# Kernel tuning notes

Hardware: AMD Instinct MI355X
Metric: run time of the kernel (lower is better)

## Reference

```python
import jax, jax.numpy as jnp
import numpy as np

N_NODES = 50000
N_EDGES = 500000
F_IN = 128
HID = 160      # hidden_sf * model_dim = 5 * 32
F_OUT = 128    # out_sf * output_channels = 4 * 32
N_GRAPHS = 50
OUT_DIM = 10


def setup_inputs() -> dict:
    key = jax.random.key(0)
    ks = jax.random.split(key, 16)
    x = jax.random.normal(ks[0], (N_NODES, F_IN), dtype=jnp.float32)
    edge_index = jax.random.randint(ks[1], (2, N_EDGES), 0, N_NODES, dtype=jnp.int64)
    batch = jnp.sort(jax.random.randint(ks[2], (N_NODES,), 0, N_GRAPHS, dtype=jnp.int64))

    def lin(k, fi, fo):
        return jax.random.normal(k, (fi, fo), dtype=jnp.float32) * (1.0 / np.sqrt(fi))

    dims = [(F_IN, HID), (HID, HID), (HID, HID), (HID, F_OUT)]
    params = {}
    for i, (fi, fo) in enumerate(dims):
        params[f"W{i}"] = lin(ks[3 + i], fi, fo)
        params[f"b{i}"] = jnp.zeros((fo,), dtype=jnp.float32)
    params["fc_w"] = lin(ks[8], F_OUT, OUT_DIM)
    params["fc_b"] = jnp.zeros((OUT_DIM,), dtype=jnp.float32)
    return {"x": x, "edge_index": edge_index, "batch": batch, **params}


def _gcn_layer(x, W, b, src, dst, dinv):
    # PyG GCNConv (improved=True): x' = D^{-1/2}(A + 2I)D^{-1/2} X W + b
    xw = x @ W                                   # [N, F_out]
    norm = dinv[src] * dinv[dst]                 # [E]
    msgs = xw[src] * norm[:, None]               # [E, F_out] gather
    agg = jax.ops.segment_sum(msgs, dst, num_segments=N_NODES)  # scatter-add
    # self-loop contribution with fill value 2 (improved)
    agg = agg + (2.0 * dinv * dinv)[:, None] * xw
    return agg + b


def reference(x, edge_index, batch, W0, b0, W1, b1, W2, b2, W3, b3, fc_w, fc_b):
    src, dst = edge_index[0], edge_index[1]
    ones_e = jnp.ones((N_EDGES,), dtype=x.dtype)
    deg = jax.ops.segment_sum(ones_e, dst, num_segments=N_NODES) + 2.0
    dinv = jax.lax.rsqrt(deg)

    h = x
    for (W, b) in [(W0, b0), (W1, b1), (W2, b2), (W3, b3)]:
        h = _gcn_layer(h, W, b, src, dst, dinv)

    # global mean pool per graph
    sums = jax.ops.segment_sum(h, batch, num_segments=N_GRAPHS)        # [G, F_OUT]
    cnts = jax.ops.segment_sum(jnp.ones((N_NODES,), h.dtype), batch, num_segments=N_GRAPHS)
    pooled = sums / jnp.maximum(cnts, 1.0)[:, None]

    logits = pooled @ fc_w + fc_b
    return jax.nn.log_softmax(logits, axis=1)
```

## Files before the change

kernel.cpp:

```cpp
#include <hip/hip_runtime.h>

#define N_NODES 50000
#define N_EDGES 500000
#define F_IN    128
#define HID     160
#define NG      50
#define OUT_DIM 10
#define PC      16
#define MAXDEG  48
#define PADK    164
#define FSTRIDE 132

#define NRANGE  8
#define RNODES  (N_NODES / NRANGE)
#define FILLB   64
#define NPACK   (N_EDGES / 4)

#define XF_ROWS   32
#define XF_BLOCKS  ((N_NODES + XF_ROWS - 1) / XF_ROWS)
#define DINV_BLOCKS ((N_NODES + 255) / 256)

__global__ void k_pre(const int* __restrict__ src, const int* __restrict__ dst,
                      int* __restrict__ deg, int* __restrict__ ell,
                      const float* __restrict__ W0, const float* __restrict__ b0,
                      const float* __restrict__ W1, const float* __restrict__ b1,
                      const float* __restrict__ W2, const float* __restrict__ b2,
                      const float* __restrict__ W3, const float* __restrict__ b3,
                      const float* __restrict__ fcw, const int* __restrict__ batch,
                      float* __restrict__ Fmt, float* __restrict__ r0,
                      float* __restrict__ r1, float* __restrict__ r2,
                      float* __restrict__ r3, int* __restrict__ start) {
    const int t = threadIdx.x;
    if (blockIdx.x >= 2) {
        const int rb    = blockIdx.x - 2;
        const int range = rb & (NRANGE - 1);
        const int sub   = rb >> 3;
        const int lo    = range * RNODES;
        const int4* d4 = (const int4*)dst;
        const int4* s4 = (const int4*)src;
        for (int pk = sub * 256 + t; pk < NPACK; pk += FILLB * 256) {
            const int4 dv = d4[pk];
            const int4 sv = s4[pk];
            #pragma unroll
            for (int j = 0; j < 4; ++j) {
                const int d = (&dv.x)[j];
                if ((unsigned)(d - lo) < (unsigned)RNODES) {
                    int p = atomicAdd(&deg[d], 1);
                    if (p < MAXDEG) ell[d * MAXDEG + p] = (&sv.x)[j];
                }
            }
        }
        return;
    }
    if (blockIdx.x == 1) {
        int g = t;
        if (g > NG) return;
        int lo = 0, hi = N_NODES;
        while (lo < hi) {
            int mid = (lo + hi) >> 1;
            if (batch[mid] < g) lo = mid + 1; else hi = mid;
        }
        start[g] = lo;
        return;
    }
    __shared__ float sA[OUT_DIM * PADK];
    __shared__ float sB[OUT_DIM * PADK];
    float* cur = sA;
    float* nxt = sB;

    for (int idx = t; idx < F_IN * OUT_DIM; idx += 256) {
        int k = idx / OUT_DIM, c = idx - k * OUT_DIM;
        cur[c * PADK + k] = fcw[idx];
    }
    __syncthreads();
    if (t < OUT_DIM) {
        float acc = 0.f;
        const float4* Bv = (const float4*)b3;
        for (int k4 = 0; k4 < F_IN / 4; ++k4) {
            float4 w = Bv[k4];
            float4 b = *(const float4*)&cur[t * PADK + 4 * k4];
            acc += w.x * b.x + w.y * b.y + w.z * b.z + w.w * b.w;
        }
        r3[t] = acc;
    }
    __syncthreads();

    auto stage = [&](const float* __restrict__ W, const float* __restrict__ bias,
                     float* __restrict__ biasOut, int M, int K, bool toGlobal) {
        const int r = t;
        const bool isBias = (r == M) && (bias != nullptr);
        if (r < M || isBias) {
            const float* Arow = isBias ? bias : (W + r * K);
            const float4* Wv = (const float4*)Arow;
            float acc[OUT_DIM];
            #pragma unroll
            for (int c = 0; c < OUT_DIM; ++c) acc[c] = 0.f;
            #pragma unroll 4
            for (int k4 = 0; k4 < K / 4; ++k4) {
                float4 w = Wv[k4];
                #pragma unroll
                for (int c = 0; c < OUT_DIM; ++c) {
                    float4 b = *(const float4*)&cur[c * PADK + 4 * k4];
                    acc[c] += w.x * b.x + w.y * b.y + w.z * b.z + w.w * b.w;
                }
            }
            if (isBias) {
                #pragma unroll
                for (int c = 0; c < OUT_DIM; ++c) biasOut[c] = acc[c];
            } else if (toGlobal) {
                #pragma unroll
                for (int c = 0; c < OUT_DIM; ++c) Fmt[c * FSTRIDE + r] = acc[c];
            } else {
                #pragma unroll
                for (int c = 0; c < OUT_DIM; ++c) nxt[c * PADK + r] = acc[c];
            }
        }
        __syncthreads();
        float* tmp = cur; cur = nxt; nxt = tmp;
    };

    stage(W3, nullptr, nullptr, HID, F_IN, false);
    stage(W2, b2, r2, HID, HID, false);
    stage(W1, b1, r1, HID, HID, false);
    stage(W0, b0, r0, F_IN, HID, true);
}

__global__ void k_xf_dinv(const float* __restrict__ X, const float* __restrict__ Fmt,
                          const int* __restrict__ deg,
                          float* __restrict__ Y0, float* __restrict__ dinv) {
    const int t = threadIdx.x;
    if (blockIdx.x >= XF_BLOCKS) {
        int i = (blockIdx.x - XF_BLOCKS) * 256 + t;
        if (i < N_NODES) dinv[i] = rsqrtf((float)deg[i] + 2.0f);
        return;
    }
    __shared__ float sX[XF_ROWS][132];
    __shared__ float sFt[OUT_DIM * FSTRIDE];
    const int base = blockIdx.x * XF_ROWS;
    for (int idx = t; idx < XF_ROWS * F_IN; idx += 256) {
        int rr = idx >> 7, kk = idx & 127;
        int gr = base + rr;
        sX[rr][kk] = (gr < N_NODES) ? X[(size_t)gr * F_IN + kk] : 0.f;
    }
    for (int idx = t; idx < OUT_DIM * FSTRIDE; idx += 256) sFt[idx] = Fmt[idx];
    __syncthreads();
    const int r = t >> 4, c = t & 15;
    float a0 = 0.f, a1 = 0.f;
    if (c < OUT_DIM) {
        for (int k = 0; k < F_IN; k += 4) {
            const float4 x0 = *(const float4*)&sX[r][k];
            const float4 x1 = *(const float4*)&sX[r + 16][k];
            const float4 f  = *(const float4*)&sFt[c * FSTRIDE + k];
            a0 += x0.x * f.x + x0.y * f.y + x0.z * f.z + x0.w * f.w;
            a1 += x1.x * f.x + x1.y * f.y + x1.z * f.z + x1.w * f.w;
        }
    }
    const float pad = (c == 10) ? 1.0f : 0.0f;
    const float v0 = (c < OUT_DIM) ? a0 : pad;
    const float v1 = (c < OUT_DIM) ? a1 : pad;
    const int g0 = base + r, g1 = base + r + 16;
    if (g0 < N_NODES) Y0[(size_t)g0 * PC + c] = v0;
    if (g1 < N_NODES) Y0[(size_t)g1 * PC + c] = v1;
}

__global__ void k_prop16(const float* __restrict__ in, const float* __restrict__ dinv,
                         const int* __restrict__ deg, const int* __restrict__ ell,
                         float* __restrict__ out) {
    const int gid  = blockIdx.x * blockDim.x + threadIdx.x;
    const int i    = gid >> 6;
    const int lane = threadIdx.x & 63;
    const int esub = lane >> 4, c = lane & 15;
    int d = deg[i];
    const int dc = (d < MAXDEG) ? d : MAXDEG;
    float acc = 0.f;
    const int base = i * MAXDEG;
    for (int k = esub; k < dc; k += 4) {
        int s = ell[base + k];
        acc += dinv[s] * in[(size_t)s * PC + c];
    }
    acc += __shfl_xor(acc, 16);
    acc += __shfl_xor(acc, 32);
    if (lane < 16) {
        float di = dinv[i];
        out[(size_t)i * PC + c] = di * (acc + 2.0f * di * in[(size_t)i * PC + c]);
    }
}

__global__ void k_pool_final(const float* __restrict__ Y1, const float* __restrict__ Y2,
                             const float* __restrict__ Y3, const float* __restrict__ Y4,
                             const int* __restrict__ start,
                             const float* __restrict__ r0, const float* __restrict__ r1,
                             const float* __restrict__ r2, const float* __restrict__ r3,
                             const float* __restrict__ fcb, float* __restrict__ out) {
    const int g = blockIdx.x, t = threadIdx.x;
    __shared__ float red[256];
    __shared__ float S_sh[16];
    __shared__ float qsh[3];
    __shared__ float lg[OUT_DIM];
    const int st = start[g], cnt = start[g + 1] - st;
    const int c = t & 15, rr = t >> 4;

    float acc = 0.f;
    for (int r = rr; r < cnt; r += 16) acc += Y4[(size_t)(st + r) * PC + c];
    red[t] = acc; __syncthreads();
    if (t < 128) red[t] += red[t + 128]; __syncthreads();
    if (t < 64)  red[t] += red[t + 64];  __syncthreads();
    if (t < 32)  red[t] += red[t + 32];  __syncthreads();
    if (t < 16)  S_sh[t] = red[t] + red[t + 16];

    float a1 = 0.f, a2 = 0.f, a3 = 0.f;
    for (int r = t; r < cnt; r += 256) {
        a1 += Y1[(size_t)(st + r) * PC + 10];
        a2 += Y2[(size_t)(st + r) * PC + 10];
        a3 += Y3[(size_t)(st + r) * PC + 10];
    }
    __syncthreads(); red[t] = a1; __syncthreads();
    for (int o = 128; o > 0; o >>= 1) { if (t < o) red[t] += red[t + o]; __syncthreads(); }
    if (t == 0) qsh[0] = red[0];
    __syncthreads(); red[t] = a2; __syncthreads();
    for (int o = 128; o > 0; o >>= 1) { if (t < o) red[t] += red[t + o]; __syncthreads(); }
    if (t == 0) qsh[1] = red[0];
    __syncthreads(); red[t] = a3; __syncthreads();
    for (int o = 128; o > 0; o >>= 1) { if (t < o) red[t] += red[t + o]; __syncthreads(); }
    if (t == 0) qsh[2] = red[0];
    __syncthreads();

    if (t < OUT_DIM) {
        float n = (float)cnt; if (n < 1.f) n = 1.f;
        lg[t] = (S_sh[t] + qsh[2] * r0[t] + qsh[1] * r1[t] + qsh[0] * r2[t]) / n
                + r3[t] + fcb[t];
    }
    __syncthreads();
    if (t == 0) {
        float m = -1e30f;
        for (int o = 0; o < OUT_DIM; ++o) m = fmaxf(m, lg[o]);
        float ss = 0.f;
        for (int o = 0; o < OUT_DIM; ++o) ss += expf(lg[o] - m);
        float ls = logf(ss) + m;
        for (int o = 0; o < OUT_DIM; ++o) out[g * OUT_DIM + o] = lg[o] - ls;
    }
}

extern "C" void kernel_launch(void* const* d_in, const int* in_sizes, int n_in,
                              void* d_out, int out_size, void* d_ws, size_t ws_size,
                              hipStream_t stream) {
    const float* x     = (const float*)d_in[0];
    const int*   ei    = (const int*)d_in[1];
    const int*   src   = ei;
    const int*   dstp  = ei + N_EDGES;
    const int*   batch = (const int*)d_in[2];
    const float* W0 = (const float*)d_in[3];
    const float* b0 = (const float*)d_in[4];
    const float* W1 = (const float*)d_in[5];
    const float* b1 = (const float*)d_in[6];
    const float* W2 = (const float*)d_in[7];
    const float* b2 = (const float*)d_in[8];
    const float* W3 = (const float*)d_in[9];
    const float* b3 = (const float*)d_in[10];
    const float* fcw = (const float*)d_in[11];
    const float* fcb = (const float*)d_in[12];
    float* out = (float*)d_out;

    char* p = (char*)d_ws;
    auto alloc = [&](size_t bytes) -> void* {
        void* r = (void*)p;
        p += (bytes + 255) & ~(size_t)255;
        return r;
    };
    int*   deg   = (int*)alloc(N_NODES * 4);
    int*   start = (int*)alloc((NG + 1) * 4);
    float* dinv  = (float*)alloc(N_NODES * 4);
    int*   ell   = (int*)alloc((size_t)N_NODES * MAXDEG * 4);
    float* Fmt   = (float*)alloc(OUT_DIM * FSTRIDE * 4);
    float* r0    = (float*)alloc(OUT_DIM * 4);
    float* r1    = (float*)alloc(OUT_DIM * 4);
    float* r2    = (float*)alloc(OUT_DIM * 4);
    float* r3    = (float*)alloc(OUT_DIM * 4);
    float* Y0    = (float*)alloc((size_t)N_NODES * PC * 4);
    float* Y1    = (float*)alloc((size_t)N_NODES * PC * 4);
    float* Y2    = (float*)alloc((size_t)N_NODES * PC * 4);
    float* Y3    = (float*)alloc((size_t)N_NODES * PC * 4);
    float* Y4    = (float*)alloc((size_t)N_NODES * PC * 4);

    hipMemsetAsync(deg, 0, N_NODES * 4, stream);

    const int TB = 256;
    k_pre<<<NRANGE * FILLB + 2, TB, 0, stream>>>(src, dstp, deg, ell,
                                                 W0, b0, W1, b1, W2, b2, W3, b3,
                                                 fcw, batch, Fmt, r0, r1, r2, r3, start);
    k_xf_dinv<<<XF_BLOCKS + DINV_BLOCKS, TB, 0, stream>>>(x, Fmt, deg, Y0, dinv);

    const int PROP_BLOCKS = N_NODES * 64 / TB;
    k_prop16<<<PROP_BLOCKS, TB, 0, stream>>>(Y0, dinv, deg, ell, Y1);
    k_prop16<<<PROP_BLOCKS, TB, 0, stream>>>(Y1, dinv, deg, ell, Y2);
    k_prop16<<<PROP_BLOCKS, TB, 0, stream>>>(Y2, dinv, deg, ell, Y3);
    k_prop16<<<PROP_BLOCKS, TB, 0, stream>>>(Y3, dinv, deg, ell, Y4);

    k_pool_final<<<NG, TB, 0, stream>>>(Y1, Y2, Y3, Y4, start, r0, r1, r2, r3, fcb, out);
}
```

Before: 258.4 us.

## Restructure pre-pass: fold memset into init kernel, fuse ELL fill with X transform, recompute dinv

```diff
diff --git a/kernel.cpp b/kernel.cpp
--- a/kernel.cpp
+++ b/kernel.cpp
@@ -13,26 +13,109 @@
 
 #define NRANGE  8
 #define RNODES  (N_NODES / NRANGE)
-#define FILLB   64
+#define FILLB   128
+#define FB      (NRANGE * FILLB)
 #define NPACK   (N_EDGES / 4)
 
 #define XF_ROWS   32
-#define XF_BLOCKS  ((N_NODES + XF_ROWS - 1) / XF_ROWS)
-#define DINV_BLOCKS ((N_NODES + 255) / 256)
-
-__global__ void k_pre(const int* __restrict__ src, const int* __restrict__ dst,
-                      int* __restrict__ deg, int* __restrict__ ell,
-                      const float* __restrict__ W0, const float* __restrict__ b0,
-                      const float* __restrict__ W1, const float* __restrict__ b1,
-                      const float* __restrict__ W2, const float* __restrict__ b2,
-                      const float* __restrict__ W3, const float* __restrict__ b3,
-                      const float* __restrict__ fcw, const int* __restrict__ batch,
-                      float* __restrict__ Fmt, float* __restrict__ r0,
-                      float* __restrict__ r1, float* __restrict__ r2,
-                      float* __restrict__ r3, int* __restrict__ start) {
+#define XF_BLOCKS ((N_NODES + XF_ROWS - 1) / XF_ROWS)
+#define ZERO_BLOCKS ((N_NODES + 255) / 256)
+
+__global__ void k_init(const float* __restrict__ W0, const float* __restrict__ b0,
+                       const float* __restrict__ W1, const float* __restrict__ b1,
+                       const float* __restrict__ W2, const float* __restrict__ b2,
+                       const float* __restrict__ W3, const float* __restrict__ b3,
+                       const float* __restrict__ fcw, const int* __restrict__ batch,
+                       float* __restrict__ Fmt, float* __restrict__ r0,
+                       float* __restrict__ r1, float* __restrict__ r2,
+                       float* __restrict__ r3, int* __restrict__ start,
+                       int* __restrict__ deg) {
     const int t = threadIdx.x;
     if (blockIdx.x >= 2) {
-        const int rb    = blockIdx.x - 2;
+        int i = (blockIdx.x - 2) * 256 + t;
+        if (i < N_NODES) deg[i] = 0;
+        return;
+    }
+    if (blockIdx.x == 1) {
+        int g = t;
+        if (g > NG) return;
+        int lo = 0, hi = N_NODES;
+        while (lo < hi) {
+            int mid = (lo + hi) >> 1;
+            if (batch[mid] < g) lo = mid + 1; else hi = mid;
+        }
+        start[g] = lo;
+        return;
+    }
+    __shared__ float sA[OUT_DIM * PADK];
+    __shared__ float sB[OUT_DIM * PADK];
+    float* cur = sA;
+    float* nxt = sB;
+
+    for (int idx = t; idx < F_IN * OUT_DIM; idx += 256) {
+        int k = idx / OUT_DIM, c = idx - k * OUT_DIM;
+        cur[c * PADK + k] = fcw[idx];
+    }
+    __syncthreads();
+    if (t < OUT_DIM) {
+        float acc = 0.f;
+        const float4* Bv = (const float4*)b3;
+        for (int k4 = 0; k4 < F_IN / 4; ++k4) {
+            float4 w = Bv[k4];
+            float4 b = *(const float4*)&cur[t * PADK + 4 * k4];
+            acc += w.x * b.x + w.y * b.y + w.z * b.z + w.w * b.w;
+        }
+        r3[t] = acc;
+    }
+    __syncthreads();
+
+    auto stage = [&](const float* __restrict__ W, const float* __restrict__ bias,
+                     float* __restrict__ biasOut, int M, int K, bool toGlobal) {
+        const int r = t;
+        const bool isBias = (r == M) && (bias != nullptr);
+        if (r < M || isBias) {
+            const float* Arow = isBias ? bias : (W + r * K);
+            const float4* Wv = (const float4*)Arow;
+            float acc[OUT_DIM];
+            #pragma unroll
+            for (int c = 0; c < OUT_DIM; ++c) acc[c] = 0.f;
+            #pragma unroll 4
+            for (int k4 = 0; k4 < K / 4; ++k4) {
+                float4 w = Wv[k4];
+                #pragma unroll
+                for (int c = 0; c < OUT_DIM; ++c) {
+                    float4 b = *(const float4*)&cur[c * PADK + 4 * k4];
+                    acc[c] += w.x * b.x + w.y * b.y + w.z * b.z + w.w * b.w;
+                }
+            }
+            if (isBias) {
+                #pragma unroll
+                for (int c = 0; c < OUT_DIM; ++c) biasOut[c] = acc[c];
+            } else if (toGlobal) {
+                #pragma unroll
+                for (int c = 0; c < OUT_DIM; ++c) Fmt[c * FSTRIDE + r] = acc[c];
+            } else {
+                #pragma unroll
+                for (int c = 0; c < OUT_DIM; ++c) nxt[c * PADK + r] = acc[c];
+            }
+        }
+        __syncthreads();
+        float* tmp = cur; cur = nxt; nxt = tmp;
+    };
+
+    stage(W3, nullptr, nullptr, HID, F_IN, false);
+    stage(W2, b2, r2, HID, HID, false);
+    stage(W1, b1, r1, HID, HID, false);
+    stage(W0, b0, r0, F_IN, HID, true);
+}
+
+__global__ void k_fill_xf(const int* __restrict__ src, const int* __restrict__ dst,
+                          int* __restrict__ deg, int* __restrict__ ell,
+                          const float* __restrict__ X, const float* __restrict__ Fmt,
+                          float* __restrict__ Y0) {
+    const int t = threadIdx.x;
+    if (blockIdx.x < FB) {
+        const int rb    = blockIdx.x;
         const int range = rb & (NRANGE - 1);
         const int sub   = rb >> 3;
         const int lo    = range * RNODES;
@@ -52,91 +135,9 @@
         }
         return;
     }
-    if (blockIdx.x == 1) {
-        int g = t;
-        if (g > NG) return;
-        int lo = 0, hi = N_NODES;
-        while (lo < hi) {
-            int mid = (lo + hi) >> 1;
-            if (batch[mid] < g) lo = mid + 1; else hi = mid;
-        }
-        start[g] = lo;
-        return;
-    }
-    __shared__ float sA[OUT_DIM * PADK];
-    __shared__ float sB[OUT_DIM * PADK];
-    float* cur = sA;
-    float* nxt = sB;
-
-    for (int idx = t; idx < F_IN * OUT_DIM; idx += 256) {
-        int k = idx / OUT_DIM, c = idx - k * OUT_DIM;
-        cur[c * PADK + k] = fcw[idx];
-    }
-    __syncthreads();
-    if (t < OUT_DIM) {
-        float acc = 0.f;
-        const float4* Bv = (const float4*)b3;
-        for (int k4 = 0; k4 < F_IN / 4; ++k4) {
-            float4 w = Bv[k4];
-            float4 b = *(const float4*)&cur[t * PADK + 4 * k4];
-            acc += w.x * b.x + w.y * b.y + w.z * b.z + w.w * b.w;
-        }
-        r3[t] = acc;
-    }
-    __syncthreads();
-
-    auto stage = [&](const float* __restrict__ W, const float* __restrict__ bias,
-                     float* __restrict__ biasOut, int M, int K, bool toGlobal) {
-        const int r = t;
-        const bool isBias = (r == M) && (bias != nullptr);
-        if (r < M || isBias) {
-            const float* Arow = isBias ? bias : (W + r * K);
-            const float4* Wv = (const float4*)Arow;
-            float acc[OUT_DIM];
-            #pragma unroll
-            for (int c = 0; c < OUT_DIM; ++c) acc[c] = 0.f;
-            #pragma unroll 4
-            for (int k4 = 0; k4 < K / 4; ++k4) {
-                float4 w = Wv[k4];
-                #pragma unroll
-                for (int c = 0; c < OUT_DIM; ++c) {
-                    float4 b = *(const float4*)&cur[c * PADK + 4 * k4];
-                    acc[c] += w.x * b.x + w.y * b.y + w.z * b.z + w.w * b.w;
-                }
-            }
-            if (isBias) {
-                #pragma unroll
-                for (int c = 0; c < OUT_DIM; ++c) biasOut[c] = acc[c];
-            } else if (toGlobal) {
-                #pragma unroll
-                for (int c = 0; c < OUT_DIM; ++c) Fmt[c * FSTRIDE + r] = acc[c];
-            } else {
-                #pragma unroll
-                for (int c = 0; c < OUT_DIM; ++c) nxt[c * PADK + r] = acc[c];
-            }
-        }
-        __syncthreads();
-        float* tmp = cur; cur = nxt; nxt = tmp;
-    };
-
-    stage(W3, nullptr, nullptr, HID, F_IN, false);
-    stage(W2, b2, r2, HID, HID, false);
-    stage(W1, b1, r1, HID, HID, false);
-    stage(W0, b0, r0, F_IN, HID, true);
-}
-
-__global__ void k_xf_dinv(const float* __restrict__ X, const float* __restrict__ Fmt,
-                          const int* __restrict__ deg,
-                          float* __restrict__ Y0, float* __restrict__ dinv) {
-    const int t = threadIdx.x;
-    if (blockIdx.x >= XF_BLOCKS) {
-        int i = (blockIdx.x - XF_BLOCKS) * 256 + t;
-        if (i < N_NODES) dinv[i] = rsqrtf((float)deg[i] + 2.0f);
-        return;
-    }
     __shared__ float sX[XF_ROWS][132];
     __shared__ float sFt[OUT_DIM * FSTRIDE];
-    const int base = blockIdx.x * XF_ROWS;
+    const int base = (blockIdx.x - FB) * XF_ROWS;
     for (int idx = t; idx < XF_ROWS * F_IN; idx += 256) {
         int rr = idx >> 7, kk = idx & 127;
         int gr = base + rr;
@@ -163,25 +164,25 @@
     if (g1 < N_NODES) Y0[(size_t)g1 * PC + c] = v1;
 }
 
-__global__ void k_prop16(const float* __restrict__ in, const float* __restrict__ dinv,
-                         const int* __restrict__ deg, const int* __restrict__ ell,
-                         float* __restrict__ out) {
+__global__ void k_prop16(const float* __restrict__ in, const int* __restrict__ deg,
+                         const int* __restrict__ ell, float* __restrict__ out) {
     const int gid  = blockIdx.x * blockDim.x + threadIdx.x;
     const int i    = gid >> 6;
     const int lane = threadIdx.x & 63;
     const int esub = lane >> 4, c = lane & 15;
-    int d = deg[i];
+    const int d = deg[i];
     const int dc = (d < MAXDEG) ? d : MAXDEG;
     float acc = 0.f;
     const int base = i * MAXDEG;
     for (int k = esub; k < dc; k += 4) {
         int s = ell[base + k];
-        acc += dinv[s] * in[(size_t)s * PC + c];
+        float ds = rsqrtf((float)deg[s] + 2.0f);
+        acc += ds * in[(size_t)s * PC + c];
     }
     acc += __shfl_xor(acc, 16);
     acc += __shfl_xor(acc, 32);
     if (lane < 16) {
-        float di = dinv[i];
+        float di = rsqrtf((float)d + 2.0f);
         out[(size_t)i * PC + c] = di * (acc + 2.0f * di * in[(size_t)i * PC + c]);
     }
 }
@@ -269,7 +270,6 @@
     };
     int*   deg   = (int*)alloc(N_NODES * 4);
     int*   start = (int*)alloc((NG + 1) * 4);
-    float* dinv  = (float*)alloc(N_NODES * 4);
     int*   ell   = (int*)alloc((size_t)N_NODES * MAXDEG * 4);
     float* Fmt   = (float*)alloc(OUT_DIM * FSTRIDE * 4);
     float* r0    = (float*)alloc(OUT_DIM * 4);
@@ -282,19 +282,17 @@
     float* Y3    = (float*)alloc((size_t)N_NODES * PC * 4);
     float* Y4    = (float*)alloc((size_t)N_NODES * PC * 4);
 
-    hipMemsetAsync(deg, 0, N_NODES * 4, stream);
-
     const int TB = 256;
-    k_pre<<<NRANGE * FILLB + 2, TB, 0, stream>>>(src, dstp, deg, ell,
-                                                 W0, b0, W1, b1, W2, b2, W3, b3,
-                                                 fcw, batch, Fmt, r0, r1, r2, r3, start);
-    k_xf_dinv<<<XF_BLOCKS + DINV_BLOCKS, TB, 0, stream>>>(x, Fmt, deg, Y0, dinv);
+    k_init<<<ZERO_BLOCKS + 2, TB, 0, stream>>>(W0, b0, W1, b1, W2, b2, W3, b3,
+                                               fcw, batch, Fmt, r0, r1, r2, r3,
+                                               start, deg);
+    k_fill_xf<<<FB + XF_BLOCKS, TB, 0, stream>>>(src, dstp, deg, ell, x, Fmt, Y0);
 
     const int PROP_BLOCKS = N_NODES * 64 / TB;
-    k_prop16<<<PROP_BLOCKS, TB, 0, stream>>>(Y0, dinv, deg, ell, Y1);
-    k_prop16<<<PROP_BLOCKS, TB, 0, stream>>>(Y1, dinv, deg, ell, Y2);
-    k_prop16<<<PROP_BLOCKS, TB, 0, stream>>>(Y2, dinv, deg, ell, Y3);
-    k_prop16<<<PROP_BLOCKS, TB, 0, stream>>>(Y3, dinv, deg, ell, Y4);
+    k_prop16<<<PROP_BLOCKS, TB, 0, stream>>>(Y0, deg, ell, Y1);
+    k_prop16<<<PROP_BLOCKS, TB, 0, stream>>>(Y1, deg, ell, Y2);
+    k_prop16<<<PROP_BLOCKS, TB, 0, stream>>>(Y2, deg, ell, Y3);
+    k_prop16<<<PROP_BLOCKS, TB, 0, stream>>>(Y3, deg, ell, Y4);
 
     k_pool_final<<<NG, TB, 0, stream>>>(Y1, Y2, Y3, Y4, start, r0, r1, r2, r3, fcb, out);
 }
```

New measurement: 264.6 us. +2.4%, slower.
